# Optimization experiments

Measured on AMD Instinct MI355X. Metric: run time of the kernel, lower is better.

The kernel has to match this reference:

```python
import jax, jax.numpy as jnp
import numpy as np

HIDDEN = 1024
INTER = 256
N_EXPERTS = 16
B, T = 4, 2048
NEG_INF = -1000000000.0


def setup_inputs() -> dict:
    key = jax.random.key(0)
    ks = jax.random.split(key, 5)
    hidden_states = jax.random.normal(ks[0], (B, T, HIDDEN), dtype=jnp.float32)
    sim_matrix = jax.random.normal(ks[1], (HIDDEN, N_EXPERTS), dtype=jnp.float32)
    threshold = jnp.zeros((1,), dtype=jnp.float32)
    # torch Linear weights: w1 [I, C], w2 [C, I]; store per-expert stacked in
    # matmul-friendly layout: w1 [E, C, I], w2 [E, I, C]
    w1 = jax.random.normal(ks[2], (N_EXPERTS, HIDDEN, INTER), dtype=jnp.float32) / np.sqrt(HIDDEN)
    w2 = jax.random.normal(ks[3], (N_EXPERTS, INTER, HIDDEN), dtype=jnp.float32) / np.sqrt(INTER)
    return {"hidden_states": hidden_states, "sim_matrix": sim_matrix,
            "threshold": threshold, "w1": w1, "w2": w2}


def _l2norm(x, axis):
    return x / jnp.maximum(jnp.linalg.norm(x, axis=axis, keepdims=True), 1e-12)


def reference(hidden_states, sim_matrix, threshold, w1, w2):
    Bq, Tq, C = hidden_states.shape
    x = hidden_states.reshape(-1, C)                      # [N, C]
    # gate
    scores = _l2norm(x, -1) @ _l2norm(sim_matrix, 0)      # [N, E]
    activated = scores > threshold
    k_per_token = activated.sum(axis=-1)                  # [N] int
    masked = jnp.where(activated, scores, NEG_INF)
    routing_weights = jax.nn.softmax(masked, axis=-1)     # [N, E]
    # dense all-expert FFN
    h = jax.nn.gelu(jnp.einsum('nc,eci->nei', x, w1), approximate=False)
    out = jnp.einsum('nei,eic->nec', h, w2)               # [N, E, C]
    final = jnp.einsum('nec,ne->nc', out, routing_weights)
    return final.reshape(Bq, Tq, C), scores, k_per_token
```

## Files before the change

kernel.cpp:

```cpp
#include <hip/hip_runtime.h>
#include <hip/hip_bf16.h>
#include <math.h>

#define NTOK 8192
#define HID  1024
#define ISZ  256
#define NEXP 16
#define NBIG 4096

typedef __attribute__((ext_vector_type(8))) short bf16x8;
typedef __attribute__((ext_vector_type(4))) float f32x4;

__device__ __forceinline__ unsigned short f2bf(float f) {
  unsigned u = __float_as_uint(f);
  u += 0x7fff + ((u >> 16) & 1);
  return (unsigned short)(u >> 16);
}

__device__ __forceinline__ void async16(void* l, const void* g) {
  __builtin_amdgcn_global_load_lds(
      (const __attribute__((address_space(1))) unsigned int*)g,
      (__attribute__((address_space(3))) unsigned int*)l, 16, 0, 0);
}

__global__ void simnorm_kernel(const float* __restrict__ sm, float* __restrict__ inv_smn) {
  __shared__ float red[16][17];
  int t = threadIdx.x;
  int e = t & 15, g = t >> 4;
  float ss = 0.f;
  for (int c = g; c < HID; c += 16) {
    float v = sm[c * NEXP + e];
    ss += v * v;
  }
  red[e][g] = ss;
  __syncthreads();
  if (t < 16) {
    float s = 0.f;
    #pragma unroll
    for (int i = 0; i < 16; i++) s += red[t][i];
    inv_smn[t] = 1.f / fmaxf(sqrtf(s), 1e-12f);
  }
}

__global__ __launch_bounds__(256)
void gate_kernel(const float* __restrict__ x, const float* __restrict__ sm,
                 const float* __restrict__ thr, const float* __restrict__ inv_smn,
                 float* __restrict__ scores_out, float* __restrict__ k_out,
                 float* __restrict__ rw_out, unsigned short* __restrict__ xb_out) {
  const int n = blockIdx.x;
  const int t = threadIdx.x;
  const int lane = t & 63, wave = t >> 6;
  const float* xr = x + (size_t)n * HID;

  float p[16];
  #pragma unroll
  for (int e = 0; e < 16; e++) p[e] = 0.f;
  float ss = 0.f;

  #pragma unroll
  for (int q = 0; q < 4; q++) {
    int c = t + q * 256;
    float v = xr[c];
    ss += v * v;
    xb_out[(size_t)n * HID + c] = f2bf(v);
    const float4* smr = (const float4*)(sm + (size_t)c * NEXP);
    float4 s0 = smr[0], s1 = smr[1], s2 = smr[2], s3 = smr[3];
    p[0] += v * s0.x;  p[1] += v * s0.y;  p[2] += v * s0.z;  p[3] += v * s0.w;
    p[4] += v * s1.x;  p[5] += v * s1.y;  p[6] += v * s1.z;  p[7] += v * s1.w;
    p[8] += v * s2.x;  p[9] += v * s2.y;  p[10] += v * s2.z; p[11] += v * s2.w;
    p[12] += v * s3.x; p[13] += v * s3.y; p[14] += v * s3.z; p[15] += v * s3.w;
  }

  #pragma unroll
  for (int off = 32; off > 0; off >>= 1) {
    ss += __shfl_down(ss, off, 64);
    #pragma unroll
    for (int e = 0; e < 16; e++) p[e] += __shfl_down(p[e], off, 64);
  }

  __shared__ float red[4][17];
  __shared__ float sc[16];
  if (lane == 0) {
    red[wave][0] = ss;
    #pragma unroll
    for (int e = 0; e < 16; e++) red[wave][1 + e] = p[e];
  }
  __syncthreads();

  if (t < 16) {
    float d = red[0][1 + t] + red[1][1 + t] + red[2][1 + t] + red[3][1 + t];
    float ssum = red[0][0] + red[1][0] + red[2][0] + red[3][0];
    float inv_x = 1.f / fmaxf(sqrtf(ssum), 1e-12f);
    float s = d * inv_x * inv_smn[t];
    scores_out[(size_t)n * 16 + t] = s;
    sc[t] = s;
  }
  __syncthreads();

  if (t < 16) {
    float thrv = thr[0];
    float s = sc[t];
    bool act = s > thrv;
    float m = act ? s : -INFINITY;
    int cnt = act ? 1 : 0;
    #pragma unroll
    for (int off = 8; off > 0; off >>= 1) {
      m = fmaxf(m, __shfl_xor(m, off, 16));
      cnt += __shfl_xor(cnt, off, 16);
    }
    float pv;
    if (cnt > 0) pv = act ? expf(s - m) : 0.f;
    else         pv = 1.f;
    float sum = pv;
    #pragma unroll
    for (int off = 8; off > 0; off >>= 1) sum += __shfl_xor(sum, off, 16);
    rw_out[(size_t)n * 16 + t] = pv / sum;
    if (t == 0) k_out[n] = (float)cnt;
  }
}

__global__ __launch_bounds__(256)
void transpose_cast_kernel(const float* __restrict__ src, unsigned short* __restrict__ dst,
                           int R, int C, int dstride, int e_src_stride, int e_dst_mult) {
  __shared__ float tile[32][33];
  const int e = blockIdx.z;
  const int r0 = blockIdx.y * 32, c0 = blockIdx.x * 32;
  const int tx = threadIdx.x & 31, ty = threadIdx.x >> 5;
  const float* s = src + (size_t)e * e_src_stride;
  #pragma unroll
  for (int q = 0; q < 4; q++) {
    int r = r0 + ty + q * 8;
    tile[ty + q * 8][tx] = s[(size_t)r * C + c0 + tx];
  }
  __syncthreads();
  unsigned short* d = dst + (size_t)e * e_dst_mult;
  #pragma unroll
  for (int q = 0; q < 4; q++) {
    int cc = c0 + ty + q * 8;
    int r  = r0 + tx;
    d[(size_t)cc * dstride + r] = f2bf(tile[tx][ty + q * 8]);
  }
}

#define G1PHASE(CK, STG, WAIT_)                                                \
  {                                                                            \
    bf16x8 afr[8], bfr[4];                                                     \
    _Pragma("unroll")                                                          \
    for (int q = 0; q < 2; q++)                                                \
      _Pragma("unroll")                                                        \
      for (int ml = 0; ml < 4; ml++)                                           \
        afr[q*4+ml] = *(const bf16x8*)(bufA + q*16384 + wmo + ml*2048 + lro + (CK)); \
    _Pragma("unroll")                                                          \
    for (int qn = 0; qn < 2; qn++)                                             \
      _Pragma("unroll")                                                        \
      for (int nl = 0; nl < 2; nl++)                                           \
        bfr[qn*2+nl] = *(const bf16x8*)(bufB + qn*16384 + wno + nl*2048 + lro + (CK)); \
    if (STG) {                                                                 \
      _Pragma("unroll")                                                        \
      for (int i = 0; i < 2; i++) {                                            \
        async16(ldsAn + o16[i],         Ag + (size_t)aRow[i]*LD + kn + aCol[i]);      \
        async16(ldsBn + o16[i],         Bg + (size_t)bRow[i]*LD + kn + bCol[i]);      \
        async16(ldsBn + 16384 + o16[i], Bg + (size_t)(bRow[i]+32)*LD + kn + bCol[i]); \
        async16(ldsAn + 16384 + o16[i], Ag + (size_t)(aRow[i]+64)*LD + kn + aCol[i]); \
      }                                                                        \
    }                                                                          \
    __builtin_amdgcn_sched_barrier(0);                                         \
    __builtin_amdgcn_s_barrier();                                              \
    asm volatile("s_waitcnt lgkmcnt(0)" ::: "memory");                         \
    __builtin_amdgcn_sched_barrier(0);                                         \
    __builtin_amdgcn_s_setprio(1);                                             \
    _Pragma("unroll")                                                          \
    for (int m8 = 0; m8 < 8; m8++)                                             \
      _Pragma("unroll")                                                        \
      for (int n4 = 0; n4 < 4; n4++)                                           \
        acc[m8][n4] = __builtin_amdgcn_mfma_f32_16x16x32_bf16(                 \
            afr[m8], bfr[n4], acc[m8][n4], 0, 0, 0);                           \
    __builtin_amdgcn_s_setprio(0);                                             \
    __builtin_amdgcn_sched_barrier(0);                                         \
    if (WAIT_) { asm volatile("s_waitcnt vmcnt(0)" ::: "memory"); }            \
    __builtin_amdgcn_s_barrier();                                              \
    __builtin_amdgcn_sched_barrier(0);                                         \
  }

template <int KEXT, int LD, int NBN>
__global__ __launch_bounds__(512, 2)
void gemm1_k(const unsigned short* __restrict__ A, const unsigned short* __restrict__ B,
             unsigned short* __restrict__ Cb, const float* __restrict__ rw) {
  __shared__ __align__(1024) char lds[131072];
  constexpr int NT = KEXT / 64;
  const int tid = threadIdx.x;
  const int lane = tid & 63, wid = tid >> 6;
  const int wm = wid >> 2, wn = wid & 3;
  const int lr = lane & 15;

  const int nwg = gridDim.x;
  const int cpx = nwg >> 3;
  int wg = (blockIdx.x & 7) * cpx + (blockIdx.x >> 3);
  const int bm = wg / NBN, bn = wg % NBN;

  const int swz = (lr & 7) << 4;
  const int colk0 = ((lane >> 4) * 16) ^ swz;
  const int colk1 = (64 + (lane >> 4) * 16) ^ swz;
  const int wmo = wm * 8192, wno = wn * 4096, lro = lr * 128;

  int aRow[2], aCol[2], bRow[2], bCol[2], o16[2];
  #pragma unroll
  for (int i = 0; i < 2; i++) {
    int o = (i * 512 + tid) * 16;
    o16[i] = o;
    { int wmb = o >> 13, ob = o & 8191, r = ob >> 7, cb = ob & 127;
      aRow[i] = wmb * 128 + r; aCol[i] = (cb ^ ((r & 7) << 4)) >> 1; }
    { int wnb = o >> 12, ob = o & 4095, r = ob >> 7, cb = ob & 127;
      bRow[i] = wnb * 64 + r; bCol[i] = (cb ^ ((r & 7) << 4)) >> 1; }
  }

  const unsigned short* Ag = A + (size_t)bm * 256 * LD;
  const unsigned short* Bg = B + (size_t)bn * 256 * LD;

  f32x4 acc[8][4];
  #pragma unroll
  for (int m = 0; m < 8; m++)
    #pragma unroll
    for (int n = 0; n < 4; n++) acc[m][n] = (f32x4){0.f, 0.f, 0.f, 0.f};

  #pragma unroll
  for (int i = 0; i < 2; i++) async16(lds + o16[i],                 Ag + (size_t)aRow[i] * LD + aCol[i]);
  #pragma unroll
  for (int i = 0; i < 2; i++) async16(lds + 65536 + o16[i],         Bg + (size_t)bRow[i] * LD + bCol[i]);
  #pragma unroll
  for (int i = 0; i < 2; i++) async16(lds + 65536 + 16384 + o16[i], Bg + (size_t)(bRow[i] + 32) * LD + bCol[i]);
  #pragma unroll
  for (int i = 0; i < 2; i++) async16(lds + 16384 + o16[i],         Ag + (size_t)(aRow[i] + 64) * LD + aCol[i]);
  asm volatile("s_waitcnt vmcnt(0)" ::: "memory");
  __builtin_amdgcn_s_barrier();

  #pragma unroll 1
  for (int t = 0; t < NT; t += 2) {
    {
      const char* bufA = lds;
      const char* bufB = lds + 65536;
      char* ldsAn = lds + 32768;
      char* ldsBn = lds + 65536 + 32768;
      const int kn = ((t + 1) & (NT - 1)) << 6;
      G1PHASE(colk0, 1, 0)
      G1PHASE(colk1, 0, 1)
    }
    {
      const char* bufA = lds + 32768;
      const char* bufB = lds + 65536 + 32768;
      char* ldsAn = lds;
      char* ldsBn = lds + 65536;
      const int kn = ((t + 2) & (NT - 1)) << 6;
      G1PHASE(colk0, 1, 0)
      G1PHASE(colk1, 0, 1)
    }
  }

  asm volatile("s_waitcnt vmcnt(0)" ::: "memory");

  const int jr = (lane >> 4) * 4;
  float wrow[8][4];
  #pragma unroll
  for (int m = 0; m < 8; m++)
    #pragma unroll
    for (int j = 0; j < 4; j++)
      wrow[m][j] = rw[(size_t)(bm * 256 + wm * 128 + m * 16 + jr + j) * 16 + bn];
  #pragma unroll
  for (int m = 0; m < 8; m++) {
    #pragma unroll
    for (int n = 0; n < 4; n++) {
      int col = bn * 256 + wn * 64 + n * 16 + lr;
      #pragma unroll
      for (int j = 0; j < 4; j++) {
        int r = bm * 256 + wm * 128 + m * 16 + jr + j;
        float v = acc[m][n][j];
        float g = 0.7978845608f * (v + 0.044715f * v * v * v);
        float e = __expf(2.f * g);
        float th = 1.f - 2.f / (e + 1.f);
        float ge = 0.5f * v * (1.f + th);
        Cb[(size_t)r * NBIG + col] = f2bf(ge * wrow[m][j]);
      }
    }
  }
}

#define G2PHASE(CK, STG, WAIT_)                                                \
  {                                                                            \
    bf16x8 afr[4], bfr[4];                                                     \
    _Pragma("unroll")                                                          \
    for (int ml = 0; ml < 4; ml++)                                             \
      afr[ml] = *(const bf16x8*)(bufA + wmo + ml*2048 + lro + (CK));           \
    _Pragma("unroll")                                                          \
    for (int nl = 0; nl < 4; nl++)                                             \
      bfr[nl] = *(const bf16x8*)(bufB + wno + nl*2048 + lro + (CK));           \
    if (STG) {                                                                 \
      _Pragma("unroll")                                                        \
      for (int i = 0; i < 2; i++)                                              \
        async16(ldsAn + o16[i], Ag + (size_t)aRow[i]*K + kn + aCol[i]);        \
      _Pragma("unroll")                                                        \
      for (int i = 0; i < 4; i++)                                              \
        async16(ldsBn + o16b[i], Bg + (size_t)bRow[i]*K + kn + bCol[i]);       \
    }                                                                          \
    __builtin_amdgcn_sched_barrier(0);                                         \
    __builtin_amdgcn_s_barrier();                                              \
    asm volatile("s_waitcnt lgkmcnt(0)" ::: "memory");                         \
    __builtin_amdgcn_sched_barrier(0);                                         \
    __builtin_amdgcn_s_setprio(1);                                             \
    _Pragma("unroll")                                                          \
    for (int m4 = 0; m4 < 4; m4++)                                             \
      _Pragma("unroll")                                                        \
      for (int n4 = 0; n4 < 4; n4++)                                           \
        acc[m4][n4] = __builtin_amdgcn_mfma_f32_16x16x32_bf16(                 \
            afr[m4], bfr[n4], acc[m4][n4], 0, 0, 0);                           \
    __builtin_amdgcn_s_setprio(0);                                             \
    __builtin_amdgcn_sched_barrier(0);                                         \
    if (WAIT_) { asm volatile("s_waitcnt vmcnt(0)" ::: "memory"); }            \
    __builtin_amdgcn_s_barrier();                                              \
    __builtin_amdgcn_sched_barrier(0);                                         \
  }

template <int K>
__global__ __launch_bounds__(512, 2)
void gemm2_k(const unsigned short* __restrict__ A, const unsigned short* __restrict__ B,
             float* __restrict__ Cf) {
  __shared__ __align__(1024) char lds[98304];
  constexpr int NT = K / 64;
  const int tid = threadIdx.x;
  const int lane = tid & 63, wid = tid >> 6;
  const int wm = wid >> 2, wn = wid & 3;
  const int lr = lane & 15;

  const int wg = (blockIdx.x & 7) * 32 + (blockIdx.x >> 3);
  const int bm = wg >> 2, bn = wg & 3;

  const int swz = (lr & 7) << 4;
  const int colk0 = ((lane >> 4) * 16) ^ swz;
  const int colk1 = (64 + (lane >> 4) * 16) ^ swz;
  const int wmo = wm * 8192, wno = wn * 8192, lro = lr * 128;

  int aRow[2], aCol[2], o16[2];
  int bRow[4], bCol[4], o16b[4];
  #pragma unroll
  for (int i = 0; i < 2; i++) {
    int o = (i * 512 + tid) * 16;
    o16[i] = o;
    int r = o >> 7, cb = o & 127;
    aRow[i] = r; aCol[i] = (cb ^ ((r & 7) << 4)) >> 1;
  }
  #pragma unroll
  for (int i = 0; i < 4; i++) {
    int o = (i * 512 + tid) * 16;
    o16b[i] = o;
    int r = o >> 7, cb = o & 127;
    bRow[i] = r; bCol[i] = (cb ^ ((r & 7) << 4)) >> 1;
  }

  const unsigned short* Ag = A + (size_t)bm * 128 * K;
  const unsigned short* Bg = B + (size_t)bn * 256 * K;

  f32x4 acc[4][4];
  #pragma unroll
  for (int m = 0; m < 4; m++)
    #pragma unroll
    for (int n = 0; n < 4; n++) acc[m][n] = (f32x4){0.f, 0.f, 0.f, 0.f};

  #pragma unroll
  for (int i = 0; i < 2; i++) async16(lds + o16[i],          Ag + (size_t)aRow[i] * K + aCol[i]);
  #pragma unroll
  for (int i = 0; i < 4; i++) async16(lds + 32768 + o16b[i], Bg + (size_t)bRow[i] * K + bCol[i]);
  asm volatile("s_waitcnt vmcnt(0)" ::: "memory");
  __builtin_amdgcn_s_barrier();

  #pragma unroll 1
  for (int t = 0; t < NT; t += 2) {
    {
      const char* bufA = lds;
      const char* bufB = lds + 32768;
      char* ldsAn = lds + 16384;
      char* ldsBn = lds + 32768 + 32768;
      const int kn = ((t + 1) & (NT - 1)) << 6;
      G2PHASE(colk0, 1, 0)
      G2PHASE(colk1, 0, 1)
    }
    {
      const char* bufA = lds + 16384;
      const char* bufB = lds + 32768 + 32768;
      char* ldsAn = lds;
      char* ldsBn = lds + 32768;
      const int kn = ((t + 2) & (NT - 1)) << 6;
      G2PHASE(colk0, 1, 0)
      G2PHASE(colk1, 0, 1)
    }
  }

  asm volatile("s_waitcnt vmcnt(0)" ::: "memory");

  const int jr = (lane >> 4) * 4;
  #pragma unroll
  for (int m = 0; m < 4; m++) {
    #pragma unroll
    for (int n = 0; n < 4; n++) {
      int col = bn * 256 + wn * 64 + n * 16 + lr;
      #pragma unroll
      for (int j = 0; j < 4; j++) {
        int r = bm * 128 + wm * 64 + m * 16 + jr + j;
        Cf[(size_t)r * HID + col] = acc[m][n][j];
      }
    }
  }
}

extern "C" void kernel_launch(void* const* d_in, const int* in_sizes, int n_in,
                              void* d_out, int out_size, void* d_ws, size_t ws_size,
                              hipStream_t stream) {
  const float* x   = (const float*)d_in[0];
  const float* sm  = (const float*)d_in[1];
  const float* thr = (const float*)d_in[2];
  const float* w1  = (const float*)d_in[3];
  const float* w2  = (const float*)d_in[4];

  float* out_final  = (float*)d_out;
  float* out_scores = out_final + (size_t)NTOK * HID;
  float* out_k      = out_scores + (size_t)NTOK * NEXP;

  char* ws = (char*)d_ws;
  size_t off = 0;
  float* inv_smn = (float*)(ws + off); off += 256;
  float* rwbuf   = (float*)(ws + off); off += (size_t)NTOK * NEXP * 4;
  unsigned short* Xb  = (unsigned short*)(ws + off); off += (size_t)NTOK * HID * 2;
  unsigned short* W1T = (unsigned short*)(ws + off); off += (size_t)NBIG * HID * 2;
  unsigned short* W2T = (unsigned short*)(ws + off); off += (size_t)HID * NBIG * 2;
  unsigned short* H   = (unsigned short*)(ws + off); off += (size_t)NTOK * NBIG * 2;

  simnorm_kernel<<<1, 256, 0, stream>>>(sm, inv_smn);
  gate_kernel<<<NTOK, 256, 0, stream>>>(x, sm, thr, inv_smn, out_scores, out_k, rwbuf, Xb);
  transpose_cast_kernel<<<dim3(ISZ / 32, HID / 32, NEXP), 256, 0, stream>>>(
      w1, W1T, HID, ISZ, HID, HID * ISZ, ISZ * HID);
  transpose_cast_kernel<<<dim3(HID / 32, ISZ / 32, NEXP), 256, 0, stream>>>(
      w2, W2T, ISZ, HID, NBIG, ISZ * HID, ISZ);

  gemm1_k<HID, HID, 16><<<512, 512, 0, stream>>>(Xb, W1T, H, rwbuf);
  gemm2_k<NBIG><<<256, 512, 0, stream>>>(H, W2T, out_final);
}
```

Measured before the change: 221.0 us.

## Load GEMM1 B operand directly from global into registers, bypassing LDS

The first expert GEMM no longer stages its weight (B) tile through shared memory. Each wave loads its own B fragments straight from global memory into registers and double-buffers them there, while only the activation (A) tile still goes through LDS via async loads. This halves LDS usage to 64 KB and removes the LDS write/read traffic and the intra-phase barriers for B. The cost is more VGPRs, global loads that may be less coalesced, and waits now tied to vmcnt counts.

```diff
diff --git a/kernel.cpp b/kernel.cpp
--- a/kernel.cpp
+++ b/kernel.cpp
@@ -10,6 +10,8 @@
 
 typedef __attribute__((ext_vector_type(8))) short bf16x8;
 typedef __attribute__((ext_vector_type(4))) float f32x4;
+
+#define MFMA16(a, b, c) __builtin_amdgcn_mfma_f32_16x16x32_bf16(a, b, c, 0, 0, 0)
 
 __device__ __forceinline__ unsigned short f2bf(float f) {
   unsigned u = __float_as_uint(f);
@@ -142,80 +144,60 @@
   }
 }
 
-#define G1PHASE(CK, STG, WAIT_)                                                \
-  {                                                                            \
-    bf16x8 afr[8], bfr[4];                                                     \
-    _Pragma("unroll")                                                          \
-    for (int q = 0; q < 2; q++)                                                \
-      _Pragma("unroll")                                                        \
-      for (int ml = 0; ml < 4; ml++)                                           \
-        afr[q*4+ml] = *(const bf16x8*)(bufA + q*16384 + wmo + ml*2048 + lro + (CK)); \
-    _Pragma("unroll")                                                          \
-    for (int qn = 0; qn < 2; qn++)                                             \
-      _Pragma("unroll")                                                        \
-      for (int nl = 0; nl < 2; nl++)                                           \
-        bfr[qn*2+nl] = *(const bf16x8*)(bufB + qn*16384 + wno + nl*2048 + lro + (CK)); \
-    if (STG) {                                                                 \
-      _Pragma("unroll")                                                        \
-      for (int i = 0; i < 2; i++) {                                            \
-        async16(ldsAn + o16[i],         Ag + (size_t)aRow[i]*LD + kn + aCol[i]);      \
-        async16(ldsBn + o16[i],         Bg + (size_t)bRow[i]*LD + kn + bCol[i]);      \
-        async16(ldsBn + 16384 + o16[i], Bg + (size_t)(bRow[i]+32)*LD + kn + bCol[i]); \
-        async16(ldsAn + 16384 + o16[i], Ag + (size_t)(aRow[i]+64)*LD + kn + aCol[i]); \
-      }                                                                        \
-    }                                                                          \
-    __builtin_amdgcn_sched_barrier(0);                                         \
-    __builtin_amdgcn_s_barrier();                                              \
-    asm volatile("s_waitcnt lgkmcnt(0)" ::: "memory");                         \
-    __builtin_amdgcn_sched_barrier(0);                                         \
-    __builtin_amdgcn_s_setprio(1);                                             \
-    _Pragma("unroll")                                                          \
-    for (int m8 = 0; m8 < 8; m8++)                                             \
-      _Pragma("unroll")                                                        \
-      for (int n4 = 0; n4 < 4; n4++)                                           \
-        acc[m8][n4] = __builtin_amdgcn_mfma_f32_16x16x32_bf16(                 \
-            afr[m8], bfr[n4], acc[m8][n4], 0, 0, 0);                           \
-    __builtin_amdgcn_s_setprio(0);                                             \
-    __builtin_amdgcn_sched_barrier(0);                                         \
-    if (WAIT_) { asm volatile("s_waitcnt vmcnt(0)" ::: "memory"); }            \
-    __builtin_amdgcn_s_barrier();                                              \
-    __builtin_amdgcn_sched_barrier(0);                                         \
+#define G1_LOADB(dst, kt)                                                       \
+  _Pragma("unroll")                                                             \
+  for (int nl = 0; nl < 4; nl++) {                                              \
+    _Pragma("unroll")                                                           \
+    for (int h = 0; h < 2; h++)                                                 \
+      dst[nl][h] = *(const bf16x8*)(Bg2 + (size_t)(kt) * 128 + nl * (LD * 32) + h * 64); \
+  }
+
+#define G1_COMPUTE(bufA, bb)                                                    \
+  _Pragma("unroll")                                                             \
+  for (int kk = 0; kk < 2; kk++) {                                              \
+    const int ck = kk ? colk1 : colk0;                                          \
+    bf16x8 a[8];                                                                \
+    _Pragma("unroll")                                                           \
+    for (int mf = 0; mf < 8; mf++)                                              \
+      a[mf] = *(const bf16x8*)((bufA) + wmo + mf * 2048 + lro + ck);            \
+    _Pragma("unroll")                                                           \
+    for (int mf = 0; mf < 8; mf++)                                              \
+      _Pragma("unroll")                                                         \
+      for (int nf = 0; nf < 4; nf++)                                            \
+        acc[mf][nf] = MFMA16(a[mf], bb[nf][kk], acc[mf][nf]);                   \
   }
 
 template <int KEXT, int LD, int NBN>
 __global__ __launch_bounds__(512, 2)
-void gemm1_k(const unsigned short* __restrict__ A, const unsigned short* __restrict__ B,
-             unsigned short* __restrict__ Cb, const float* __restrict__ rw) {
-  __shared__ __align__(1024) char lds[131072];
+void gemm1_bd(const unsigned short* __restrict__ A, const unsigned short* __restrict__ B,
+              unsigned short* __restrict__ Cb, const float* __restrict__ rw) {
+  __shared__ __align__(1024) char lds[65536];
   constexpr int NT = KEXT / 64;
   const int tid = threadIdx.x;
   const int lane = tid & 63, wid = tid >> 6;
   const int wm = wid >> 2, wn = wid & 3;
   const int lr = lane & 15;
 
-  const int nwg = gridDim.x;
-  const int cpx = nwg >> 3;
-  int wg = (blockIdx.x & 7) * cpx + (blockIdx.x >> 3);
+  const int nwg = gridDim.x, cpx = nwg >> 3;
+  const int wg = (blockIdx.x & 7) * cpx + (blockIdx.x >> 3);
   const int bm = wg / NBN, bn = wg % NBN;
 
   const int swz = (lr & 7) << 4;
   const int colk0 = ((lane >> 4) * 16) ^ swz;
   const int colk1 = (64 + (lane >> 4) * 16) ^ swz;
-  const int wmo = wm * 8192, wno = wn * 4096, lro = lr * 128;
-
-  int aRow[2], aCol[2], bRow[2], bCol[2], o16[2];
-  #pragma unroll
-  for (int i = 0; i < 2; i++) {
+  const int wmo = wm * 16384, lro = lr * 128;
+
+  int sRow[4], sCol[4], so[4];
+  #pragma unroll
+  for (int i = 0; i < 4; i++) {
     int o = (i * 512 + tid) * 16;
-    o16[i] = o;
-    { int wmb = o >> 13, ob = o & 8191, r = ob >> 7, cb = ob & 127;
-      aRow[i] = wmb * 128 + r; aCol[i] = (cb ^ ((r & 7) << 4)) >> 1; }
-    { int wnb = o >> 12, ob = o & 4095, r = ob >> 7, cb = ob & 127;
-      bRow[i] = wnb * 64 + r; bCol[i] = (cb ^ ((r & 7) << 4)) >> 1; }
+    so[i] = o;
+    int r = o >> 7, cb = o & 127;
+    sRow[i] = r; sCol[i] = (cb ^ ((r & 7) << 4)) >> 1;
   }
 
   const unsigned short* Ag = A + (size_t)bm * 256 * LD;
-  const unsigned short* Bg = B + (size_t)bn * 256 * LD;
+  const char* Bg2 = (const char*)(B + (size_t)(bn * 256 + wn * 64 + lr) * LD) + ((lane >> 4) * 16);
 
   f32x4 acc[8][4];
   #pragma unroll
@@ -223,36 +205,46 @@
     #pragma unroll
     for (int n = 0; n < 4; n++) acc[m][n] = (f32x4){0.f, 0.f, 0.f, 0.f};
 
-  #pragma unroll
-  for (int i = 0; i < 2; i++) async16(lds + o16[i],                 Ag + (size_t)aRow[i] * LD + aCol[i]);
-  #pragma unroll
-  for (int i = 0; i < 2; i++) async16(lds + 65536 + o16[i],         Bg + (size_t)bRow[i] * LD + bCol[i]);
-  #pragma unroll
-  for (int i = 0; i < 2; i++) async16(lds + 65536 + 16384 + o16[i], Bg + (size_t)(bRow[i] + 32) * LD + bCol[i]);
-  #pragma unroll
-  for (int i = 0; i < 2; i++) async16(lds + 16384 + o16[i],         Ag + (size_t)(aRow[i] + 64) * LD + aCol[i]);
-  asm volatile("s_waitcnt vmcnt(0)" ::: "memory");
+  bf16x8 b0[4][2], b1[4][2];
+
+  #pragma unroll
+  for (int i = 0; i < 4; i++) async16(lds + so[i], Ag + (size_t)sRow[i] * LD + sCol[i]);
+  __builtin_amdgcn_sched_barrier(0);
+  G1_LOADB(b0, 0)
+  __builtin_amdgcn_sched_barrier(0);
+  asm volatile("s_waitcnt vmcnt(8)" ::: "memory");
   __builtin_amdgcn_s_barrier();
+  __builtin_amdgcn_sched_barrier(0);
 
   #pragma unroll 1
   for (int t = 0; t < NT; t += 2) {
     {
-      const char* bufA = lds;
-      const char* bufB = lds + 65536;
-      char* ldsAn = lds + 32768;
-      char* ldsBn = lds + 65536 + 32768;
-      const int kn = ((t + 1) & (NT - 1)) << 6;
-      G1PHASE(colk0, 1, 0)
-      G1PHASE(colk1, 0, 1)
+      const int kn = (t + 1) & (NT - 1);
+      #pragma unroll
+      for (int i = 0; i < 4; i++)
+        async16(lds + 32768 + so[i], Ag + (size_t)sRow[i] * LD + kn * 64 + sCol[i]);
+      __builtin_amdgcn_sched_barrier(0);
+      G1_LOADB(b1, kn)
+      __builtin_amdgcn_sched_barrier(0);
+      G1_COMPUTE(lds, b0)
+      __builtin_amdgcn_sched_barrier(0);
+      asm volatile("s_waitcnt vmcnt(8)" ::: "memory");
+      __builtin_amdgcn_s_barrier();
+      __builtin_amdgcn_sched_barrier(0);
     }
     {
-      const char* bufA = lds + 32768;
-      const char* bufB = lds + 65536 + 32768;
-      char* ldsAn = lds;
-      char* ldsBn = lds + 65536;
-      const int kn = ((t + 2) & (NT - 1)) << 6;
-      G1PHASE(colk0, 1, 0)
-      G1PHASE(colk1, 0, 1)
+      const int kn = (t + 2) & (NT - 1);
+      #pragma unroll
+      for (int i = 0; i < 4; i++)
+        async16(lds + so[i], Ag + (size_t)sRow[i] * LD + kn * 64 + sCol[i]);
+      __builtin_amdgcn_sched_barrier(0);
+      G1_LOADB(b0, kn)
+      __builtin_amdgcn_sched_barrier(0);
+      G1_COMPUTE(lds + 32768, b1)
+      __builtin_amdgcn_sched_barrier(0);
+      asm volatile("s_waitcnt vmcnt(8)" ::: "memory");
+      __builtin_amdgcn_s_barrier();
+      __builtin_amdgcn_sched_barrier(0);
     }
   }
 
@@ -310,8 +302,7 @@
     for (int m4 = 0; m4 < 4; m4++)                                             \
       _Pragma("unroll")                                                        \
       for (int n4 = 0; n4 < 4; n4++)                                           \
-        acc[m4][n4] = __builtin_amdgcn_mfma_f32_16x16x32_bf16(                 \
-            afr[m4], bfr[n4], acc[m4][n4], 0, 0, 0);                           \
+        acc[m4][n4] = MFMA16(afr[m4], bfr[n4], acc[m4][n4]);                   \
     __builtin_amdgcn_s_setprio(0);                                             \
     __builtin_amdgcn_sched_barrier(0);                                         \
     if (WAIT_) { asm volatile("s_waitcnt vmcnt(0)" ::: "memory"); }            \
@@ -439,6 +430,6 @@
   transpose_cast_kernel<<<dim3(HID / 32, ISZ / 32, NEXP), 256, 0, stream>>>(
       w2, W2T, ISZ, HID, NBIG, ISZ * HID, ISZ);
 
-  gemm1_k<HID, HID, 16><<<512, 512, 0, stream>>>(Xb, W1T, H, rwbuf);
+  gemm1_bd<HID, HID, 16><<<512, 512, 0, stream>>>(Xb, W1T, H, rwbuf);
   gemm2_k<NBIG><<<256, 512, 0, stream>>>(H, W2T, out_final);
 }
```

New measurement: 247.9 us. +12.2%, slower.
